# Kernel tuning notes

Measured on AMD Instinct MI355X. Metric: run time of the kernel, lower is better.

Reference implementation:

```python
import jax, jax.numpy as jnp
import numpy as np

B, S, H, D = 2, 2048, 16, 64

def setup_inputs() -> dict:
    key = jax.random.key(0)
    kq, kk, kv = jax.random.split(key, 3)
    q = jax.random.normal(kq, (B, S, H, D), dtype=jnp.float32)
    k = jax.random.normal(kk, (B, S, H, D), dtype=jnp.float32)
    v = jax.random.normal(kv, (B, S, H, D), dtype=jnp.float32)
    return {"q": q, "k": k, "v": v}

def reference(q, k, v):
    # q, k, v: [B, S, H, D]; single-process path == full softmax attention,
    # which is exactly what the ring online-softmax computes over all chunks.
    d = q.shape[-1]
    scale = 1.0 / jnp.sqrt(jnp.asarray(d, dtype=q.dtype))
    # scores: [B, H, Sq, Sk]
    scores = jnp.einsum("bqhd,bkhd->bhqk", q, k) * scale
    attn = jax.nn.softmax(scores, axis=-1)
    # output back in [B, S, H, D] layout (torch transposes back)
    out = jnp.einsum("bhqk,bkhd->bqhd", attn, v)
    return out
```

## Files before the change

### kernel.cpp

```cpp
#include <hip/hip_runtime.h>
#include <hip/hip_bf16.h>

namespace {

constexpr int Sseq = 2048;
constexpr int NH   = 16;
constexpr int HD   = 64;
constexpr int ROW  = NH * HD;
constexpr int BN   = 64;
constexpr int NT   = Sseq / BN;
constexpr int BM   = 128;
constexpr size_t IMG_BYTES = 16384;
constexpr size_t WS_NEED   = (size_t)32 * NT * IMG_BYTES;
constexpr float QSCALE = 0.18033688011112042f;

typedef __bf16 bf16_t;
typedef __attribute__((ext_vector_type(8))) bf16_t bf16x8;
typedef __attribute__((ext_vector_type(4))) float f32x4;
typedef __attribute__((ext_vector_type(16))) float f32x16;
typedef __attribute__((ext_vector_type(2))) unsigned int u32x2;
typedef __attribute__((ext_vector_type(4))) unsigned int u32x4;

union Frag { bf16x8 v; unsigned int u[4]; };

__device__ inline unsigned int pkbf(float a, float b) {
  union { __hip_bfloat162 h; unsigned int u; } x;
  x.h = __float22bfloat162_rn(make_float2(a, b));
  return x.u;
}

__device__ inline void dma16(const void* g, void* l) {
  __builtin_amdgcn_global_load_lds(
      (const __attribute__((address_space(1))) void*)g,
      (__attribute__((address_space(3))) void*)l, 16, 0, 0);
}


__global__ __launch_bounds__(256)
void prep_kv(const float* __restrict__ K, const float* __restrict__ V,
             unsigned short* __restrict__ ws) {
  const int id  = blockIdx.x;
  const int bh  = id & 31;
  const int t   = id >> 5;
  const int tid = threadIdx.x;

  const size_t base = (size_t)(bh >> 4) * Sseq * ROW + (size_t)(bh & 15) * HD
                    + (size_t)(t * BN) * ROW;
  const float* kb = K + base;
  const float* vb = V + base;

  unsigned short* gK = (unsigned short*)((char*)ws + (size_t)(bh * NT + t) * IMG_BYTES);
  unsigned short* gV = gK + 4096;

  {
    const int kr = tid >> 2;
    const int kd = (tid & 3) * 16;
    const float* p = kb + (size_t)kr * ROW + kd;
    f32x4 x0 = *(const f32x4*)(p);
    f32x4 x1 = *(const f32x4*)(p + 4);
    f32x4 x2 = *(const f32x4*)(p + 8);
    f32x4 x3 = *(const f32x4*)(p + 12);
    int c0 = ((tid & 3) * 2) ^ (kr & 7);
    int c1 = ((tid & 3) * 2 + 1) ^ (kr & 7);
    u32x4 w0, w1;
    w0.x = pkbf(x0[0], x0[1]); w0.y = pkbf(x0[2], x0[3]);
    w0.z = pkbf(x1[0], x1[1]); w0.w = pkbf(x1[2], x1[3]);
    w1.x = pkbf(x2[0], x2[1]); w1.y = pkbf(x2[2], x2[3]);
    w1.z = pkbf(x3[0], x3[1]); w1.w = pkbf(x3[2], x3[3]);
    *(u32x4*)(gK + kr * 64 + c0 * 8) = w0;
    *(u32x4*)(gK + kr * 64 + c1 * 8) = w1;
  }
  {
    const int n4 = (tid & 15) * 4;
    const int d4 = (tid >> 4) * 4;
    const float* p = vb + (size_t)n4 * ROW + d4;
    f32x4 r0 = *(const f32x4*)(p);
    f32x4 r1 = *(const f32x4*)(p + ROW);
    f32x4 r2 = *(const f32x4*)(p + 2 * ROW);
    f32x4 r3 = *(const f32x4*)(p + 3 * ROW);
    #pragma unroll
    for (int i = 0; i < 4; ++i) {
      int d = d4 + i;
      int chunk = (n4 >> 3) ^ (d & 7);
      u32x2 val; val.x = pkbf(r0[i], r1[i]); val.y = pkbf(r2[i], r3[i]);
      *(u32x2*)(gV + d * 64 + chunk * 8 + (n4 & 7)) = val;
    }
  }
}

__global__ __launch_bounds__(256, 2)
void fa_main(const float* __restrict__ Q, const unsigned short* __restrict__ ws,
             float* __restrict__ O) {
  const int id   = blockIdx.x;
  const int bh   = id & 31;
  const int qblk = id >> 5;
  const int tid  = threadIdx.x;
  const int wave = tid >> 6;
  const int lane = tid & 63;
  const int wk   = wave & 1;
  const int wq   = wave >> 1;
  const int l31  = lane & 31;
  const int h    = lane >> 5;

  const size_t base = (size_t)(bh >> 4) * Sseq * ROW + (size_t)(bh & 15) * HD;
  const float* qb = Q + base;
  float*       ob = O + base;
  const char*  imgs = (const char*)ws + (size_t)bh * NT * IMG_BYTES;

  __shared__ __align__(16) unsigned char smem[32768 + 20480 + 512];
  unsigned short (*KV)[8192] = (unsigned short (*)[8192])smem;
  unsigned char* pb  = smem + 32768 + wave * 5120;
  float*         lsc = (float*)(smem + 32768 + 20480);

  const int qrow0 = qblk * BM + wq * 64;

  Frag qf[2][4];
  #pragma unroll
  for (int nt = 0; nt < 2; ++nt) {
    const float* qp = qb + (size_t)(qrow0 + nt * 32 + l31) * ROW + h * 8;
    #pragma unroll
    for (int f = 0; f < 4; ++f) {
      f32x4 a = *(const f32x4*)(qp + f * 16);
      f32x4 b = *(const f32x4*)(qp + f * 16 + 4);
      qf[nt][f].u[0] = pkbf(a[0] * QSCALE, a[1] * QSCALE);
      qf[nt][f].u[1] = pkbf(a[2] * QSCALE, a[3] * QSCALE);
      qf[nt][f].u[2] = pkbf(b[0] * QSCALE, b[1] * QSCALE);
      qf[nt][f].u[3] = pkbf(b[2] * QSCALE, b[3] * QSCALE);
    }
  }

  f32x16 oacc[2][2] = {};
  float lsum[2] = {};

  auto dma_tile = [&](int t, int b) {
    const char* img = imgs + (size_t)t * IMG_BYTES;
    char* dst = (char*)&KV[b][0];
    int woff = wave * 1024;
    #pragma unroll
    for (int j = 0; j < 4; ++j)
      dma16(img + j * 4096 + woff + lane * 16, dst + j * 4096 + woff);
  };

  dma_tile(0, 0);

  for (int t = 0; t < NT; ++t) {
    __syncthreads();
    if (t + 1 < NT) dma_tile(t + 1, (t + 1) & 1);

    const unsigned short* kt = &KV[t & 1][0];
    const unsigned short* vt = &KV[t & 1][4096];

    Frag ka[4];
    {
      int r = wk * 32 + l31;
      const unsigned short* krow = kt + r * 64;
      #pragma unroll
      for (int f = 0; f < 4; ++f) {
        int c = (2 * f + h) ^ (r & 7);
        ka[f].v = *(const bf16x8*)(krow + c * 8);
      }
    }

    #pragma unroll
    for (int nt = 0; nt < 2; ++nt) {
      f32x16 s = {};
      #pragma unroll
      for (int f = 0; f < 4; ++f)
        s = __builtin_amdgcn_mfma_f32_32x32x16_bf16(ka[f].v, qf[nt][f].v, s, 0, 0, 0);
      float e[16]; float ls = 0.f;
      #pragma unroll
      for (int i = 0; i < 16; ++i) { e[i] = __builtin_amdgcn_exp2f(s[i]); ls += e[i]; }
      lsum[nt] += ls;
      int qq = nt * 32 + l31;
      unsigned char* prow = pb + qq * 80;
      int sw = (qq >> 3) & 3;
      #pragma unroll
      for (int c2 = 0; c2 < 4; ++c2) {
        u32x2 w;
        w.x = pkbf(e[4 * c2],     e[4 * c2 + 1]);
        w.y = pkbf(e[4 * c2 + 2], e[4 * c2 + 3]);
        *(u32x2*)(prow + ((c2 ^ sw) * 16 + 8 * h)) = w;
      }
    }

    __threadfence_block();

    Frag va[2][2];
    #pragma unroll
    for (int mt = 0; mt < 2; ++mt) {
      int d = mt * 32 + l31;
      const unsigned short* vrow = vt + d * 64;
      #pragma unroll
      for (int k2 = 0; k2 < 2; ++k2) {
        int c = (4 * wk + 2 * k2 + h) ^ (d & 7);
        va[mt][k2].v = *(const bf16x8*)(vrow + c * 8);
      }
    }

    #pragma unroll
    for (int nt = 0; nt < 2; ++nt) {
      int qq = nt * 32 + l31;
      const unsigned char* prow = pb + qq * 80;
      int sw = (qq >> 3) & 3;
      #pragma unroll
      for (int k2 = 0; k2 < 2; ++k2) {
        Frag pf;
        pf.v = *(const bf16x8*)(prow + ((2 * k2 + h) ^ sw) * 16);
        #pragma unroll
        for (int mt = 0; mt < 2; ++mt)
          oacc[mt][nt] = __builtin_amdgcn_mfma_f32_32x32x16_bf16(
              va[mt][k2].v, pf.v, oacc[mt][nt], 0, 0, 0);
      }
    }
  }

  __syncthreads();
  float* osc = (float*)smem;

  #pragma unroll
  for (int nt = 0; nt < 2; ++nt) lsum[nt] += __shfl_xor(lsum[nt], 32, 64);

  if (wk == 1) {
    if (h == 0) {
      lsc[(wq * 2 + 0) * 32 + l31] = lsum[0];
      lsc[(wq * 2 + 1) * 32 + l31] = lsum[1];
    }
    float* dst = osc + wq * 4096 + lane * 64;
    #pragma unroll
    for (int nt = 0; nt < 2; ++nt)
      #pragma unroll
      for (int mt = 0; mt < 2; ++mt)
        #pragma unroll
        for (int g = 0; g < 4; ++g) {
          int idx = nt * 8 + mt * 4 + g;
          f32x4 w;
          w[0] = oacc[mt][nt][4 * g];     w[1] = oacc[mt][nt][4 * g + 1];
          w[2] = oacc[mt][nt][4 * g + 2]; w[3] = oacc[mt][nt][4 * g + 3];
          *(f32x4*)(dst + (idx ^ (lane & 15)) * 4) = w;
        }
  }
  __syncthreads();
  if (wk == 0) {
    const float* src = osc + wq * 4096 + lane * 64;
    #pragma unroll
    for (int nt = 0; nt < 2; ++nt) {
      float l = lsum[nt] + lsc[(wq * 2 + nt) * 32 + l31];
      float r = 1.0f / l;
      int q = qrow0 + nt * 32 + l31;
      float* op = ob + (size_t)q * ROW;
      #pragma unroll
      for (int mt = 0; mt < 2; ++mt)
        #pragma unroll
        for (int g = 0; g < 4; ++g) {
          int idx = nt * 8 + mt * 4 + g;
          f32x4 w = *(const f32x4*)(src + (idx ^ (lane & 15)) * 4);
          int dbase = mt * 32 + 8 * g + 4 * h;
          f32x4 o;
          o[0] = (oacc[mt][nt][4 * g]     + w[0]) * r;
          o[1] = (oacc[mt][nt][4 * g + 1] + w[1]) * r;
          o[2] = (oacc[mt][nt][4 * g + 2] + w[2]) * r;
          o[3] = (oacc[mt][nt][4 * g + 3] + w[3]) * r;
          *(f32x4*)(op + dbase) = o;
        }
    }
  }
}

__global__ __launch_bounds__(256)
void fa_fwd_fb(const float* __restrict__ Q, const float* __restrict__ K,
               const float* __restrict__ V, float* __restrict__ O) {
  constexpr int BMf = 128, MT = 2;
  const int id   = blockIdx.x;
  const int bh   = id & 31;
  const int qblk = id >> 5;
  const int tid  = threadIdx.x;
  const int wave = tid >> 6;
  const int lane = tid & 63;
  const int qd   = lane >> 4;
  const int lm   = lane & 15;

  const size_t base = (size_t)(bh >> 4) * Sseq * ROW + (size_t)(bh & 15) * HD;
  const float* qb = Q + base;
  const float* kb = K + base;
  const float* vb = V + base;
  float*       ob = O + base;

  __shared__ __align__(16) unsigned short KT[2][HD * 64];
  __shared__ __align__(16) unsigned short VT[2][HD * 64];
  __shared__ __align__(16) unsigned short PBf[4][MT][16 * 64];

  const int qrow0 = qblk * BMf + wave * (MT * 16);

  Frag qf[MT][2];
  for (int mt = 0; mt < MT; ++mt) {
    const float* qp = qb + (size_t)(qrow0 + mt * 16 + lm) * ROW;
    for (int ks = 0; ks < 2; ++ks) {
      f32x4 a = *(const f32x4*)(qp + ks * 32 + qd * 8);
      f32x4 c = *(const f32x4*)(qp + ks * 32 + qd * 8 + 4);
      qf[mt][ks].u[0] = pkbf(a[0] * QSCALE, a[1] * QSCALE);
      qf[mt][ks].u[1] = pkbf(a[2] * QSCALE, a[3] * QSCALE);
      qf[mt][ks].u[2] = pkbf(c[0] * QSCALE, c[1] * QSCALE);
      qf[mt][ks].u[3] = pkbf(c[2] * QSCALE, c[3] * QSCALE);
    }
  }

  f32x4 oacc[MT][4] = {};
  float lsum[MT] = {};

  const int kr = tid >> 2;
  const int kd = (tid & 3) * 16;
  const int n4 = (tid & 15) * 4;
  const int d4 = (tid >> 4) * 4;

  const float* kp = kb + (size_t)kr * ROW + kd;
  const float* vp = vb + (size_t)n4 * ROW + d4;

  f32x4 kx0 = *(const f32x4*)(kp);
  f32x4 kx1 = *(const f32x4*)(kp + 4);
  f32x4 kx2 = *(const f32x4*)(kp + 8);
  f32x4 kx3 = *(const f32x4*)(kp + 12);
  f32x4 vx0 = *(const f32x4*)(vp);
  f32x4 vx1 = *(const f32x4*)(vp + ROW);
  f32x4 vx2 = *(const f32x4*)(vp + 2 * ROW);
  f32x4 vx3 = *(const f32x4*)(vp + 3 * ROW);

  for (int t = 0; t < NT; ++t) {
    unsigned short* kt = KT[t & 1];
    unsigned short* vt = VT[t & 1];
    {
      int c0 = ((tid & 3) * 2) ^ (kr & 7);
      int c1 = ((tid & 3) * 2 + 1) ^ (kr & 7);
      u32x4 w0, w1;
      w0.x = pkbf(kx0[0], kx0[1]); w0.y = pkbf(kx0[2], kx0[3]);
      w0.z = pkbf(kx1[0], kx1[1]); w0.w = pkbf(kx1[2], kx1[3]);
      w1.x = pkbf(kx2[0], kx2[1]); w1.y = pkbf(kx2[2], kx2[3]);
      w1.z = pkbf(kx3[0], kx3[1]); w1.w = pkbf(kx3[2], kx3[3]);
      *(u32x4*)(kt + kr * 64 + c0 * 8) = w0;
      *(u32x4*)(kt + kr * 64 + c1 * 8) = w1;
    }
    {
      #pragma unroll
      for (int i = 0; i < 4; ++i) {
        int d = d4 + i;
        int chunk = (n4 >> 3) ^ (d & 7);
        u32x2 val; val.x = pkbf(vx0[i], vx1[i]); val.y = pkbf(vx2[i], vx3[i]);
        *(u32x2*)(vt + d * 64 + chunk * 8 + (n4 & 7)) = val;
      }
    }
    __syncthreads();
    if (t + 1 < NT) {
      kp += BN * ROW; vp += BN * ROW;
      kx0 = *(const f32x4*)(kp);
      kx1 = *(const f32x4*)(kp + 4);
      kx2 = *(const f32x4*)(kp + 8);
      kx3 = *(const f32x4*)(kp + 12);
      vx0 = *(const f32x4*)(vp);
      vx1 = *(const f32x4*)(vp + ROW);
      vx2 = *(const f32x4*)(vp + 2 * ROW);
      vx3 = *(const f32x4*)(vp + 3 * ROW);
    }
    #pragma unroll
    for (int c = 0; c < 4; ++c) {
      Frag kf0, kf1;
      {
        int r = c * 16 + lm;
        int ch0 = (qd) ^ (lm & 7);
        int ch1 = (4 + qd) ^ (lm & 7);
        kf0.v = *(const bf16x8*)(kt + r * 64 + ch0 * 8);
        kf1.v = *(const bf16x8*)(kt + r * 64 + ch1 * 8);
      }
      #pragma unroll
      for (int mt = 0; mt < MT; ++mt) {
        f32x4 s = {};
        s = __builtin_amdgcn_mfma_f32_16x16x32_bf16(kf0.v, qf[mt][0].v, s, 0, 0, 0);
        s = __builtin_amdgcn_mfma_f32_16x16x32_bf16(kf1.v, qf[mt][1].v, s, 0, 0, 0);
        float e0 = __builtin_amdgcn_exp2f(s[0]);
        float e1 = __builtin_amdgcn_exp2f(s[1]);
        float e2 = __builtin_amdgcn_exp2f(s[2]);
        float e3 = __builtin_amdgcn_exp2f(s[3]);
        lsum[mt] += (e0 + e1) + (e2 + e3);
        int n = c * 16 + qd * 4;
        int chunk = (n >> 3) ^ (lm & 7);
        u32x2 val; val.x = pkbf(e0, e1); val.y = pkbf(e2, e3);
        *(u32x2*)(PBf[wave][mt] + lm * 64 + chunk * 8 + (n & 7)) = val;
      }
    }
    __threadfence_block();
    #pragma unroll
    for (int ks = 0; ks < 2; ++ks) {
      bf16x8 pfr[MT];
      #pragma unroll
      for (int mt = 0; mt < MT; ++mt) {
        int chunk = (ks * 4 + qd) ^ (lm & 7);
        pfr[mt] = *(const bf16x8*)(PBf[wave][mt] + lm * 64 + chunk * 8);
      }
      #pragma unroll
      for (int dt = 0; dt < 4; ++dt) {
        int d = dt * 16 + lm;
        int chunk = (ks * 4 + qd) ^ (d & 7);
        bf16x8 vf = *(const bf16x8*)(vt + d * 64 + chunk * 8);
        #pragma unroll
        for (int mt = 0; mt < MT; ++mt)
          oacc[mt][dt] = __builtin_amdgcn_mfma_f32_16x16x32_bf16(vf, pfr[mt], oacc[mt][dt], 0, 0, 0);
      }
    }
  }

  #pragma unroll
  for (int mt = 0; mt < MT; ++mt) {
    float l = lsum[mt];
    l += __shfl_xor(l, 16, 64);
    l += __shfl_xor(l, 32, 64);
    float r = 1.0f / l;
    float* op = ob + (size_t)(qrow0 + mt * 16 + lm) * ROW + qd * 4;
    #pragma unroll
    for (int dt = 0; dt < 4; ++dt) {
      f32x4 o = oacc[mt][dt];
      o[0] *= r; o[1] *= r; o[2] *= r; o[3] *= r;
      *(f32x4*)(op + dt * 16) = o;
    }
  }
}

}

extern "C" void kernel_launch(void* const* d_in, const int* in_sizes, int n_in,
                              void* d_out, int out_size, void* d_ws, size_t ws_size,
                              hipStream_t stream) {
  const float* q = (const float*)d_in[0];
  const float* k = (const float*)d_in[1];
  const float* v = (const float*)d_in[2];
  float* o = (float*)d_out;
  (void)in_sizes; (void)n_in; (void)out_size;
  if (ws_size >= WS_NEED) {
    hipLaunchKernelGGL(prep_kv, dim3(32 * NT), dim3(256), 0, stream,
                       k, v, (unsigned short*)d_ws);
    hipLaunchKernelGGL(fa_main, dim3(32 * (Sseq / BM)), dim3(256), 0, stream,
                       q, (const unsigned short*)d_ws, o);
  } else {
    hipLaunchKernelGGL(fa_fwd_fb, dim3(2 * NH * (Sseq / 128)), dim3(256), 0, stream,
                       q, k, v, o);
  }
}
```

Baseline: 141.1 us.

## Load K/V tiles directly from global into registers and drop shared memory

The main attention kernel no longer stages K/V tiles in LDS through async DMA with block barriers. Each wave now owns 32 query rows and loads the full 64-key K/V tile straight from the pre-swizzled workspace into registers, double-buffered across iterations. P is rearranged into the MFMA B-operand with cross-half-wave shuffles instead of an LDS round trip. Because each wave covers all keys, the cross-wave output reduction through shared memory goes away. In exchange, every wave re-reads K/V from global/L2 (four times the traffic per block) and register pressure rises sharply with the double-buffered fragments.

```diff
diff --git a/kernel.cpp b/kernel.cpp
--- a/kernel.cpp
+++ b/kernel.cpp
@@ -9,7 +9,6 @@
 constexpr int ROW  = NH * HD;
 constexpr int BN   = 64;
 constexpr int NT   = Sseq / BN;
-constexpr int BM   = 128;
 constexpr size_t IMG_BYTES = 16384;
 constexpr size_t WS_NEED   = (size_t)32 * NT * IMG_BYTES;
 constexpr float QSCALE = 0.18033688011112042f;
@@ -27,12 +26,6 @@
   union { __hip_bfloat162 h; unsigned int u; } x;
   x.h = __float22bfloat162_rn(make_float2(a, b));
   return x.u;
-}
-
-__device__ inline void dma16(const void* g, void* l) {
-  __builtin_amdgcn_global_load_lds(
-      (const __attribute__((address_space(1))) void*)g,
-      (__attribute__((address_space(3))) void*)l, 16, 0, 0);
 }
 
 
@@ -88,182 +81,139 @@
   }
 }
 
-__global__ __launch_bounds__(256, 2)
+__global__ __launch_bounds__(256)
 void fa_main(const float* __restrict__ Q, const unsigned short* __restrict__ ws,
              float* __restrict__ O) {
-  const int id   = blockIdx.x;
-  const int bh   = id & 31;
-  const int qblk = id >> 5;
+  const int blk  = blockIdx.x;
+  const int bh   = blk & 31;
   const int tid  = threadIdx.x;
   const int wave = tid >> 6;
   const int lane = tid & 63;
-  const int wk   = wave & 1;
-  const int wq   = wave >> 1;
   const int l31  = lane & 31;
   const int h    = lane >> 5;
+  const int qt   = (blk >> 5) * 4 + wave;
 
   const size_t base = (size_t)(bh >> 4) * Sseq * ROW + (size_t)(bh & 15) * HD;
   const float* qb = Q + base;
   float*       ob = O + base;
   const char*  imgs = (const char*)ws + (size_t)bh * NT * IMG_BYTES;
 
-  __shared__ __align__(16) unsigned char smem[32768 + 20480 + 512];
-  unsigned short (*KV)[8192] = (unsigned short (*)[8192])smem;
-  unsigned char* pb  = smem + 32768 + wave * 5120;
-  float*         lsc = (float*)(smem + 32768 + 20480);
-
-  const int qrow0 = qblk * BM + wq * 64;
-
-  Frag qf[2][4];
-  #pragma unroll
-  for (int nt = 0; nt < 2; ++nt) {
-    const float* qp = qb + (size_t)(qrow0 + nt * 32 + l31) * ROW + h * 8;
+  const int qrow0 = qt * 32;
+
+  Frag qf[4];
+  {
+    const float* qp = qb + (size_t)(qrow0 + l31) * ROW + h * 8;
     #pragma unroll
     for (int f = 0; f < 4; ++f) {
       f32x4 a = *(const f32x4*)(qp + f * 16);
       f32x4 b = *(const f32x4*)(qp + f * 16 + 4);
-      qf[nt][f].u[0] = pkbf(a[0] * QSCALE, a[1] * QSCALE);
-      qf[nt][f].u[1] = pkbf(a[2] * QSCALE, a[3] * QSCALE);
-      qf[nt][f].u[2] = pkbf(b[0] * QSCALE, b[1] * QSCALE);
-      qf[nt][f].u[3] = pkbf(b[2] * QSCALE, b[3] * QSCALE);
-    }
-  }
-
-  f32x16 oacc[2][2] = {};
-  float lsum[2] = {};
-
-  auto dma_tile = [&](int t, int b) {
-    const char* img = imgs + (size_t)t * IMG_BYTES;
-    char* dst = (char*)&KV[b][0];
-    int woff = wave * 1024;
-    #pragma unroll
-    for (int j = 0; j < 4; ++j)
-      dma16(img + j * 4096 + woff + lane * 16, dst + j * 4096 + woff);
-  };
-
-  dma_tile(0, 0);
-
-  for (int t = 0; t < NT; ++t) {
-    __syncthreads();
-    if (t + 1 < NT) dma_tile(t + 1, (t + 1) & 1);
-
-    const unsigned short* kt = &KV[t & 1][0];
-    const unsigned short* vt = &KV[t & 1][4096];
-
-    Frag ka[4];
-    {
-      int r = wk * 32 + l31;
-      const unsigned short* krow = kt + r * 64;
+      qf[f].u[0] = pkbf(a[0] * QSCALE, a[1] * QSCALE);
+      qf[f].u[1] = pkbf(a[2] * QSCALE, a[3] * QSCALE);
+      qf[f].u[2] = pkbf(b[0] * QSCALE, b[1] * QSCALE);
+      qf[f].u[3] = pkbf(b[2] * QSCALE, b[3] * QSCALE);
+    }
+  }
+
+  f32x16 oacc[2] = {};
+  float lsum = 0.f;
+
+  Frag ka[2][2][4];
+  Frag va[2][2][2][2];
+
+  auto ldTile = [&](int t, int buf) {
+    const unsigned short* img = (const unsigned short*)(imgs + (size_t)t * IMG_BYTES);
+    const unsigned short* gV  = img + 4096;
+    #pragma unroll
+    for (int kh = 0; kh < 2; ++kh) {
+      int r = kh * 32 + l31;
+      const unsigned short* rowp = img + r * 64;
       #pragma unroll
       for (int f = 0; f < 4; ++f) {
         int c = (2 * f + h) ^ (r & 7);
-        ka[f].v = *(const bf16x8*)(krow + c * 8);
-      }
-    }
-
-    #pragma unroll
-    for (int nt = 0; nt < 2; ++nt) {
-      f32x16 s = {};
-      #pragma unroll
-      for (int f = 0; f < 4; ++f)
-        s = __builtin_amdgcn_mfma_f32_32x32x16_bf16(ka[f].v, qf[nt][f].v, s, 0, 0, 0);
-      float e[16]; float ls = 0.f;
-      #pragma unroll
-      for (int i = 0; i < 16; ++i) { e[i] = __builtin_amdgcn_exp2f(s[i]); ls += e[i]; }
-      lsum[nt] += ls;
-      int qq = nt * 32 + l31;
-      unsigned char* prow = pb + qq * 80;
-      int sw = (qq >> 3) & 3;
-      #pragma unroll
-      for (int c2 = 0; c2 < 4; ++c2) {
-        u32x2 w;
-        w.x = pkbf(e[4 * c2],     e[4 * c2 + 1]);
-        w.y = pkbf(e[4 * c2 + 2], e[4 * c2 + 3]);
-        *(u32x2*)(prow + ((c2 ^ sw) * 16 + 8 * h)) = w;
-      }
-    }
-
-    __threadfence_block();
-
-    Frag va[2][2];
+        ka[buf][kh][f].v = *(const bf16x8*)(rowp + c * 8);
+      }
+    }
     #pragma unroll
     for (int mt = 0; mt < 2; ++mt) {
       int d = mt * 32 + l31;
-      const unsigned short* vrow = vt + d * 64;
+      const unsigned short* rowp = gV + d * 64;
+      #pragma unroll
+      for (int kh = 0; kh < 2; ++kh)
+        #pragma unroll
+        for (int k2 = 0; k2 < 2; ++k2) {
+          int c = (4 * kh + 2 * k2 + h) ^ (d & 7);
+          va[buf][mt][kh][k2].v = *(const bf16x8*)(rowp + c * 8);
+        }
+    }
+  };
+
+  ldTile(0, 0);
+
+  for (int t = 0; t < NT; ++t) {
+    const int cur = t & 1;
+    if (t + 1 < NT) ldTile(t + 1, cur ^ 1);
+
+    #pragma unroll
+    for (int kh = 0; kh < 2; ++kh) {
+      f32x16 s = {};
+      #pragma unroll
+      for (int f = 0; f < 4; ++f)
+        s = __builtin_amdgcn_mfma_f32_32x32x16_bf16(ka[cur][kh][f].v, qf[f].v, s, 0, 0, 0);
+
+      float e[16];
+      float ls = 0.f;
+      #pragma unroll
+      for (int i = 0; i < 16; ++i) { e[i] = __builtin_amdgcn_exp2f(s[i]); ls += e[i]; }
+      lsum += ls;
+
+      unsigned int pk[4][2];
+      #pragma unroll
+      for (int c2 = 0; c2 < 4; ++c2) {
+        pk[c2][0] = pkbf(e[4 * c2],     e[4 * c2 + 1]);
+        pk[c2][1] = pkbf(e[4 * c2 + 2], e[4 * c2 + 3]);
+      }
+
+      unsigned int s0 = h ? pk[0][0] : pk[1][0];
+      unsigned int s1 = h ? pk[0][1] : pk[1][1];
+      unsigned int s2 = h ? pk[2][0] : pk[3][0];
+      unsigned int s3 = h ? pk[2][1] : pk[3][1];
+      unsigned int r0 = (unsigned int)__shfl_xor((int)s0, 32, 64);
+      unsigned int r1 = (unsigned int)__shfl_xor((int)s1, 32, 64);
+      unsigned int r2 = (unsigned int)__shfl_xor((int)s2, 32, 64);
+      unsigned int r3 = (unsigned int)__shfl_xor((int)s3, 32, 64);
+
       #pragma unroll
       for (int k2 = 0; k2 < 2; ++k2) {
-        int c = (4 * wk + 2 * k2 + h) ^ (d & 7);
-        va[mt][k2].v = *(const bf16x8*)(vrow + c * 8);
-      }
-    }
-
-    #pragma unroll
-    for (int nt = 0; nt < 2; ++nt) {
-      int qq = nt * 32 + l31;
-      const unsigned char* prow = pb + qq * 80;
-      int sw = (qq >> 3) & 3;
-      #pragma unroll
-      for (int k2 = 0; k2 < 2; ++k2) {
+        unsigned int own0 = pk[2 * k2 + h][0], own1 = pk[2 * k2 + h][1];
+        unsigned int par0 = k2 ? r2 : r0,      par1 = k2 ? r3 : r1;
         Frag pf;
-        pf.v = *(const bf16x8*)(prow + ((2 * k2 + h) ^ sw) * 16);
+        pf.u[0] = h ? par0 : own0;
+        pf.u[1] = h ? par1 : own1;
+        pf.u[2] = h ? own0 : par0;
+        pf.u[3] = h ? own1 : par1;
         #pragma unroll
         for (int mt = 0; mt < 2; ++mt)
-          oacc[mt][nt] = __builtin_amdgcn_mfma_f32_32x32x16_bf16(
-              va[mt][k2].v, pf.v, oacc[mt][nt], 0, 0, 0);
-      }
-    }
-  }
-
-  __syncthreads();
-  float* osc = (float*)smem;
-
+          oacc[mt] = __builtin_amdgcn_mfma_f32_32x32x16_bf16(
+              va[cur][mt][kh][k2].v, pf.v, oacc[mt], 0, 0, 0);
+      }
+    }
+  }
+
+  lsum += __shfl_xor(lsum, 32, 64);
+  const float r = 1.0f / lsum;
+  float* op = ob + (size_t)(qrow0 + l31) * ROW;
   #pragma unroll
-  for (int nt = 0; nt < 2; ++nt) lsum[nt] += __shfl_xor(lsum[nt], 32, 64);
-
-  if (wk == 1) {
-    if (h == 0) {
-      lsc[(wq * 2 + 0) * 32 + l31] = lsum[0];
-      lsc[(wq * 2 + 1) * 32 + l31] = lsum[1];
-    }
-    float* dst = osc + wq * 4096 + lane * 64;
-    #pragma unroll
-    for (int nt = 0; nt < 2; ++nt)
-      #pragma unroll
-      for (int mt = 0; mt < 2; ++mt)
-        #pragma unroll
-        for (int g = 0; g < 4; ++g) {
-          int idx = nt * 8 + mt * 4 + g;
-          f32x4 w;
-          w[0] = oacc[mt][nt][4 * g];     w[1] = oacc[mt][nt][4 * g + 1];
-          w[2] = oacc[mt][nt][4 * g + 2]; w[3] = oacc[mt][nt][4 * g + 3];
-          *(f32x4*)(dst + (idx ^ (lane & 15)) * 4) = w;
-        }
-  }
-  __syncthreads();
-  if (wk == 0) {
-    const float* src = osc + wq * 4096 + lane * 64;
-    #pragma unroll
-    for (int nt = 0; nt < 2; ++nt) {
-      float l = lsum[nt] + lsc[(wq * 2 + nt) * 32 + l31];
-      float r = 1.0f / l;
-      int q = qrow0 + nt * 32 + l31;
-      float* op = ob + (size_t)q * ROW;
-      #pragma unroll
-      for (int mt = 0; mt < 2; ++mt)
-        #pragma unroll
-        for (int g = 0; g < 4; ++g) {
-          int idx = nt * 8 + mt * 4 + g;
-          f32x4 w = *(const f32x4*)(src + (idx ^ (lane & 15)) * 4);
-          int dbase = mt * 32 + 8 * g + 4 * h;
-          f32x4 o;
-          o[0] = (oacc[mt][nt][4 * g]     + w[0]) * r;
-          o[1] = (oacc[mt][nt][4 * g + 1] + w[1]) * r;
-          o[2] = (oacc[mt][nt][4 * g + 2] + w[2]) * r;
-          o[3] = (oacc[mt][nt][4 * g + 3] + w[3]) * r;
-          *(f32x4*)(op + dbase) = o;
-        }
-    }
-  }
+  for (int mt = 0; mt < 2; ++mt)
+    #pragma unroll
+    for (int g = 0; g < 4; ++g) {
+      int d0 = mt * 32 + 8 * g + 4 * h;
+      f32x4 o;
+      o[0] = oacc[mt][4 * g]     * r;
+      o[1] = oacc[mt][4 * g + 1] * r;
+      o[2] = oacc[mt][4 * g + 2] * r;
+      o[3] = oacc[mt][4 * g + 3] * r;
+      *(f32x4*)(op + d0) = o;
+    }
 }
 
 __global__ __launch_bounds__(256)
@@ -435,7 +385,7 @@
   if (ws_size >= WS_NEED) {
     hipLaunchKernelGGL(prep_kv, dim3(32 * NT), dim3(256), 0, stream,
                        k, v, (unsigned short*)d_ws);
-    hipLaunchKernelGGL(fa_main, dim3(32 * (Sseq / BM)), dim3(256), 0, stream,
+    hipLaunchKernelGGL(fa_main, dim3(512), dim3(256), 0, stream,
                        q, (const unsigned short*)d_ws, o);
   } else {
     hipLaunchKernelGGL(fa_fwd_fb, dim3(2 * NH * (Sseq / 128)), dim3(256), 0, stream,
```

Result: slower. 457.7 us (+224.4%).
